# Optimization experiments

Measured on AMD Instinct MI355X. Metric: run time of the kernel, lower is better.

## Reference

```python
import jax, jax.numpy as jnp
import numpy as np

G = 32           # number of graphs
NODES = 256      # nodes per graph (equal-sized graphs)
P = 8            # primary capsules per node
IN_DIM = 128     # primary capsule dim
O = 16           # out_caps
OUT_DIM = 128    # out capsule dim
SDIM = OUT_DIM // 2
V = 16           # vector channels
R = 3            # routing iterations


def squash(t, axis=-1):
    sn = jnp.sum(t * t, axis=axis, keepdims=True)
    scale = sn / (1.0 + sn)
    return scale * t / (jnp.sqrt(sn) + 1e-8)


def setup_inputs() -> dict:
    key = jax.random.key(0)
    ks = jax.random.split(key, 4)
    N = G * NODES
    x = jax.random.normal(ks[0], (N, P, IN_DIM), dtype=jnp.float32)
    x_vectors = jax.random.normal(ks[1], (N, V, 3), dtype=jnp.float32)
    W_scalar = jax.random.normal(ks[2], (O, IN_DIM // 2, SDIM), dtype=jnp.float32)
    W_vector = jax.random.normal(ks[3], (O, IN_DIM // 2, OUT_DIM - SDIM), dtype=jnp.float32)
    bias = jnp.zeros((O, OUT_DIM), dtype=jnp.float32)
    batch = jnp.repeat(jnp.arange(G, dtype=jnp.int64), NODES)  # contiguous equal-size graphs
    return {"x": x, "x_vectors": x_vectors, "W_scalar": W_scalar,
            "W_vector": W_vector, "bias": bias, "batch": batch}


def reference(x, x_vectors, W_scalar, W_vector, bias, batch):
    # Equal-size contiguous graphs -> per-graph masking == reshape to [G, NODES, ...]
    xg = x.reshape(G, NODES, P, IN_DIM)
    xvg = x_vectors.reshape(G, NODES, V, 3)

    def per_graph(xb, xvb):
        scalar_part = xb[..., : IN_DIM // 2]           # [n, P, D/2]
        vector_part = xb[..., IN_DIM // 2:]
        u_s = jnp.einsum('npd,ods->npos', scalar_part, W_scalar)
        u_v = jnp.einsum('npd,odv->npov', vector_part, W_vector)
        u = jnp.concatenate([u_s, u_v], axis=-1).reshape(NODES * P, O, OUT_DIM)

        b = jnp.zeros((NODES * P, O), dtype=xb.dtype)
        c = None
        v = None
        for it in range(R):
            c = jax.nn.softmax(b, axis=1)                     # [M, O]
            s_j = jnp.einsum('mo,mod->od', c, u) + bias       # [O, OUT_DIM]
            v = squash(s_j, axis=1)
            if it < R - 1:
                agreement = jnp.einsum('mos,os->mo', u[..., :SDIM], v[:, :SDIM])
                b = b + agreement

        cr = c.reshape(NODES, P, O)
        routed = jnp.einsum('npo,nvc->ovc', cr, xvb)          # [O, V, 3]
        return v, routed

    caps, vecs = jax.vmap(per_graph)(xg, xvg)
    return caps, vecs
```

## Files before the change

### kernel.cpp

```cpp
#include <hip/hip_runtime.h>

#define G_    32
#define O_    16
#define OUTD  128
#define DS_   64
#define VC    48
#define M_    2048
#define ROWS  128
#define CPG   16
#define XP    136
#define XPD   68
#define WVP   72
#define XNP   72
#define YLP   132

typedef __attribute__((ext_vector_type(8))) short short8;
typedef __attribute__((ext_vector_type(4))) float f32x4;
typedef unsigned long long u64_t;

__device__ __forceinline__ unsigned short f2bf(float f) {
  unsigned u = __float_as_uint(f);
  return (unsigned short)((u + 0x7FFFu + ((u >> 16) & 1u)) >> 16);
}
__device__ __forceinline__ float bf2f(short v) {
  return __uint_as_float(((unsigned)(unsigned short)v) << 16);
}
__device__ __forceinline__ unsigned cvtpk(float lo, float hi) {
  unsigned r;
  asm("v_cvt_pk_bf16_f32 %0, %1, %2" : "=v"(r) : "v"(lo), "v"(hi));
  return r;
}

__device__ __forceinline__ void st8f(float* p, float a, float b) {
  union { float f[2]; u64_t u; } x; x.f[0] = a; x.f[1] = b;
  __hip_atomic_store((u64_t*)p, x.u, __ATOMIC_RELAXED, __HIP_MEMORY_SCOPE_AGENT);
}
__device__ __forceinline__ void ld8f(const float* p, float& a, float& b) {
  union { float f[2]; u64_t u; } x;
  x.u = __hip_atomic_load((const u64_t*)p, __ATOMIC_RELAXED, __HIP_MEMORY_SCOPE_AGENT);
  a = x.f[0]; b = x.f[1];
}

__device__ __forceinline__ void graph_barrier(unsigned* cnt, unsigned target) {
  asm volatile("s_waitcnt vmcnt(0)" ::: "memory");
  __syncthreads();
  if (threadIdx.x == 0) {
    __hip_atomic_fetch_add(cnt, 1u, __ATOMIC_RELAXED, __HIP_MEMORY_SCOPE_AGENT);
    unsigned guard = 0;
    while (__hip_atomic_load(cnt, __ATOMIC_RELAXED, __HIP_MEMORY_SCOPE_AGENT) < target) {
      __builtin_amdgcn_s_sleep(1);
      if (++guard > (1u << 20)) break;
    }
  }
  __syncthreads();
}

__global__ __launch_bounds__(512) void caps_mega7(
    const float* __restrict__ x, const float* __restrict__ xv,
    const float* __restrict__ Ws, const float* __restrict__ Wv,
    const float* __restrict__ bias, short* __restrict__ wvacc_bf,
    float* __restrict__ y_part, float* __restrict__ routed_part,
    float* __restrict__ ysum_part, float* __restrict__ caps,
    float* __restrict__ vecs, unsigned* __restrict__ bar)
{
  const int b = blockIdx.x, g = b >> 4, chunk = b & 15;
  const int t = threadIdx.x;
  const int lane = t & 63, w = t >> 6;

  __shared__ short xT[128 * XP];
  __shared__ short xN[128 * XNP];
  __shared__ short cT[O_ * XP];
  __shared__ short wv_s[O_ * WVP];
  __shared__ float y_lds[16 * YLP];
  __shared__ float cp_s[16][17];
  __shared__ float xv_s[16 * VC];
  __shared__ float yB[128];
  __shared__ float ps[2][128];
  __shared__ float vB[64];
  __shared__ float pn_s[2];
  __shared__ float wv_acc_s[64];

  unsigned* cnt = bar + g * 64;

  {
    const float* xg = x + (size_t)b * (ROWS * OUTD);
    const int rg = lane, c16 = w;
    const float* r0 = xg + (size_t)(2 * rg) * OUTD + c16 * 16;
    const float* r1 = r0 + OUTD;
    const float4* r0q = (const float4*)r0;
    const float4* r1q = (const float4*)r1;
    float4 a0 = r0q[0], a1 = r0q[1], a2 = r0q[2], a3 = r0q[3];
    float4 b0 = r1q[0], b1 = r1q[1], b2 = r1q[2], b3 = r1q[3];
    unsigned pk[16];
    pk[ 0] = cvtpk(a0.x, b0.x); pk[ 1] = cvtpk(a0.y, b0.y);
    pk[ 2] = cvtpk(a0.z, b0.z); pk[ 3] = cvtpk(a0.w, b0.w);
    pk[ 4] = cvtpk(a1.x, b1.x); pk[ 5] = cvtpk(a1.y, b1.y);
    pk[ 6] = cvtpk(a1.z, b1.z); pk[ 7] = cvtpk(a1.w, b1.w);
    pk[ 8] = cvtpk(a2.x, b2.x); pk[ 9] = cvtpk(a2.y, b2.y);
    pk[10] = cvtpk(a2.z, b2.z); pk[11] = cvtpk(a2.w, b2.w);
    pk[12] = cvtpk(a3.x, b3.x); pk[13] = cvtpk(a3.y, b3.y);
    pk[14] = cvtpk(a3.z, b3.z); pk[15] = cvtpk(a3.w, b3.w);
    unsigned* xTd = (unsigned*)xT;
    const int kb = c16 * 16;
#pragma unroll
    for (int i = 0; i < 16; ++i) xTd[(kb + i) * XPD + rg] = pk[i];
    if (c16 < 4) {
      union { unsigned u[4]; short8 s; } pA, pB;
#pragma unroll
      for (int j = 0; j < 4; ++j) {
        pA.u[j] = (pk[2*j] & 0xFFFFu) | (pk[2*j+1] << 16);
        pB.u[j] = (pk[2*j] >> 16) | (pk[2*j+1] & 0xFFFF0000u);
      }
      *(short8*)&xN[(2 * rg) * XNP + kb]     = pA.s;
      *(short8*)&xN[(2 * rg + 1) * XNP + kb] = pB.s;
#pragma unroll
      for (int j = 0; j < 4; ++j) {
        pA.u[j] = (pk[8+2*j] & 0xFFFFu) | (pk[8+2*j+1] << 16);
        pB.u[j] = (pk[8+2*j] >> 16) | (pk[8+2*j+1] & 0xFFFF0000u);
      }
      *(short8*)&xN[(2 * rg) * XNP + kb + 8]     = pA.s;
      *(short8*)&xN[(2 * rg + 1) * XNP + kb + 8] = pB.s;
    }
    float cs[16];
#pragma unroll
    for (int i = 0; i < 16; ++i)
      cs[i] = bf2f((short)(pk[i] & 0xFFFF)) + bf2f((short)(pk[i] >> 16));
#pragma unroll
    for (int i = 0; i < 16; ++i) {
      cs[i] += __shfl_xor(cs[i], 1);
      cs[i] += __shfl_xor(cs[i], 2);
      cs[i] += __shfl_xor(cs[i], 4);
      cs[i] += __shfl_xor(cs[i], 8);
      cs[i] += __shfl_xor(cs[i], 16);
      cs[i] += __shfl_xor(cs[i], 32);
    }
    if (lane == 0) {
#pragma unroll
      for (int i = 0; i < 8; ++i)
        st8f(&ysum_part[(size_t)b * 128 + kb + 2 * i], cs[2*i], cs[2*i+1]);
    }
  }
  {
    const float* xvg = xv + (size_t)(g * 256 + chunk * 16) * VC;
    for (int i = t; i < 16 * VC; i += 512) xv_s[i] = xvg[i];
  }
  graph_barrier(cnt, 16);

#define A_ROLE(LASTF)                                                          \
  {                                                                            \
    if (t < 256) {                                                             \
      u64_t v4 = __hip_atomic_load(                                            \
          (const u64_t*)&wvacc_bf[(size_t)g * 1024 + t * 4],                   \
          __ATOMIC_RELAXED, __HIP_MEMORY_SCOPE_AGENT);                         \
      const int o = t >> 4, k = (t * 4) & 63;                                  \
      wv_s[o * WVP + k + 0] = (short)(v4 & 0xFFFF);                            \
      wv_s[o * WVP + k + 1] = (short)((v4 >> 16) & 0xFFFF);                    \
      wv_s[o * WVP + k + 2] = (short)((v4 >> 32) & 0xFFFF);                    \
      wv_s[o * WVP + k + 3] = (short)((v4 >> 48) & 0xFFFF);                    \
    }                                                                          \
    __syncthreads();                                                           \
          \
    { const int mrow = lane & 15, gq = lane >> 4;                              \
      const int nt = w;                                                        \
      const int mcol = nt * 16 + mrow;                                         \
      f32x4 acc = {0.f, 0.f, 0.f, 0.f};                                        \
      _Pragma("unroll")                                                        \
      for (int ks = 0; ks < 2; ++ks) {                                         \
        short8 af = *(const short8*)&wv_s[mrow * WVP + ks * 32 + gq * 8];      \
        short8 bfr = *(const short8*)&xN[mcol * XNP + ks * 32 + gq * 8];       \
        acc = __builtin_amdgcn_mfma_f32_16x16x32_bf16(af, bfr, acc, 0, 0, 0);  \
      }                                                                        \
      float mx = fmaxf(fmaxf(acc[0], acc[1]), fmaxf(acc[2], acc[3]));          \
      mx = fmaxf(mx, __shfl_xor(mx, 16));                                      \
      mx = fmaxf(mx, __shfl_xor(mx, 32));                                      \
      float e0 = __expf(acc[0] - mx), e1 = __expf(acc[1] - mx);                \
      float e2 = __expf(acc[2] - mx), e3 = __expf(acc[3] - mx);                \
      float sm = e0 + e1 + e2 + e3;                                            \
      sm += __shfl_xor(sm, 16);                                                \
      sm += __shfl_xor(sm, 32);                                                \
      float inv = 1.f / sm;                                                    \
      float c0 = e0 * inv, c1 = e1 * inv, c2 = e2 * inv, c3 = e3 * inv;        \
      cT[(gq * 4 + 0) * XP + mcol] = (short)f2bf(c0);                          \
      cT[(gq * 4 + 1) * XP + mcol] = (short)f2bf(c1);                          \
      cT[(gq * 4 + 2) * XP + mcol] = (short)f2bf(c2);                          \
      cT[(gq * 4 + 3) * XP + mcol] = (short)f2bf(c3);                          \
      if (LASTF) {                                                             \
        float cf[4] = {c0, c1, c2, c3};                                        \
        _Pragma("unroll")                                                      \
        for (int r = 0; r < 4; ++r) {                                          \
          float v = cf[r];                                                     \
          v += __shfl_xor(v, 1); v += __shfl_xor(v, 2); v += __shfl_xor(v, 4); \
          if ((lane & 7) == 0)                                                 \
            cp_s[nt * 2 + ((lane >> 3) & 1)][gq * 4 + r] = v;                  \
        }                                                                      \
      } }                                                                      \
    __syncthreads();                                                           \
                                              \
    { const int oc = lane & 15, gq = lane >> 4;                                \
      f32x4 y0 = {0.f,0.f,0.f,0.f};                                            \
      _Pragma("unroll")                                                        \
      for (int ks = 0; ks < 4; ++ks) {                                         \
        short8 bfv = *(const short8*)&cT[oc * XP + ks * 32 + gq * 8];          \
        short8 av = *(const short8*)&xT[(w * 16 + oc) * XP + ks * 32 + gq * 8];\
        y0 = __builtin_amdgcn_mfma_f32_16x16x32_bf16(av, bfv, y0, 0, 0, 0);    \
      }                                                                        \
      _Pragma("unroll")                                                        \
      for (int r = 0; r < 4; ++r)                                              \
        y_lds[oc * YLP + w * 16 + gq * 4 + r] = y0[r]; }                       \
    __syncthreads();                                                           \
    { float* yp = y_part + (size_t)b * 2048;                                   \
      const int oo = t >> 5, kk = (t * 4) & 127;                               \
      const float* sp = &y_lds[oo * YLP + kk];                                 \
      st8f(&yp[t * 4], sp[0], sp[1]);                                          \
      st8f(&yp[t * 4 + 2], sp[2], sp[3]); }                                    \
    if (LASTF) {                                                               \
      if (t < 384) {                                                           \
        float* rp = routed_part + (size_t)b * 768;                             \
        const int idx0 = 2 * t;                                                \
        const int o = idx0 / VC, j = idx0 - o * VC;                            \
        float a0 = 0.f, a1 = 0.f;                                              \
        _Pragma("unroll")                                                      \
        for (int n = 0; n < 16; ++n) {                                         \
          a0 += cp_s[n][o] * xv_s[n * VC + j];                                 \
          a1 += cp_s[n][o] * xv_s[n * VC + j + 1];                             \
        }                                                                      \
        st8f(&rp[idx0], a0, a1);                                               \
      } }                                                                      \
  }

#define B_ROLE(FIRSTF, LASTF)                                                  \
  {                                                                            \
    const int o = chunk;                                                       \
    if (t < 64) {                                                              \
      float s0 = 0.f, s1 = 0.f;                                                \
      if (FIRSTF) {                                                            \
        _Pragma("unroll")                                                      \
        for (int ch = 0; ch < CPG; ++ch) {                                     \
          float a, bb;                                                         \
          ld8f(&ysum_part[(size_t)(g * CPG + ch) * 128 + 2 * t], a, bb);       \
          s0 += a; s1 += bb;                                                   \
        }                                                                      \
        s0 *= 0.0625f; s1 *= 0.0625f;                                          \
      } else {                                                                 \
        const float* yp = y_part + (size_t)g * CPG * 2048 + o * 128 + 2 * t;   \
        _Pragma("unroll")                                                      \
        for (int ch = 0; ch < CPG; ++ch) {                                     \
          float a, bb; ld8f(&yp[ch * 2048], a, bb);                            \
          s0 += a; s1 += bb;                                                   \
        }                                                                      \
      }                                                                        \
      yB[2*t] = s0; yB[2*t+1] = s1;                                            \
    }                                                                          \
    __syncthreads();                                                           \
    if (t < 256) {          \
      const int kh = t >> 7, d = t & 127;                                      \
      const float* W = (d < 64) ? (Ws + (size_t)o * 4096 + d)                  \
                                : (Wv + (size_t)o * 4096 + (d - 64));          \
      const int ybase = (d < 64) ? 0 : 64;                                     \
      float a0 = 0.f, a1 = 0.f;                                                \
      _Pragma("unroll")                                                        \
      for (int k = 0; k < 32; k += 2) {                                        \
        const int kl = kh * 32 + k;                                            \
        a0 += yB[ybase + kl] * W[(size_t)kl * 64];                             \
        a1 += yB[ybase + kl + 1] * W[(size_t)(kl + 1) * 64];                   \
      }                                                                        \
      ps[kh][d] = a0 + a1;                                                     \
    }                                                                          \
    __syncthreads();                                                           \
    float sv = 0.f;                                                            \
    if (t < 128) {                                                             \
      sv = ps[0][t] + ps[1][t] + bias[o * OUTD + t];                           \
      float pn = sv * sv;                                                      \
      _Pragma("unroll")                                                        \
      for (int m = 1; m < 64; m <<= 1) pn += __shfl_xor(pn, m);                \
      if ((t & 63) == 0) pn_s[t >> 6] = pn;                                    \
    }                                                                          \
    __syncthreads();                                                           \
    if (t < 128) {                                                             \
      float sn = pn_s[0] + pn_s[1];                                            \
      float f = sn / ((1.f + sn) * (sqrtf(sn) + 1e-8f));                       \
      float v = f * sv;                                                        \
      if (t < 64) vB[t] = v;                                                   \
      if (LASTF) caps[((size_t)g * O_ + o) * OUTD + t] = v;                    \
    }                                                                          \
    __syncthreads();                                                           \
    if (!(LASTF)) {                                                            \
      if (t < 128) {              \
        const int k = t >> 1, half = t & 1;                                    \
        const float* Wr = Ws + ((size_t)o * 64 + k) * 64 + half * 32;          \
        float acc = 0.f;                                                       \
        _Pragma("unroll")                                                      \
        for (int ss = 0; ss < 32; ss += 4) {                                   \
          float4 wq = *(const float4*)(Wr + ss);                               \
          float4 vq = *(const float4*)&vB[half * 32 + ss];                     \
          acc += wq.x*vq.x + wq.y*vq.y + wq.z*vq.z + wq.w*vq.w;                \
        }                                                                      \
        acc += __shfl_xor(acc, 1);                                             \
        if (half == 0)                                                         \
          wv_acc_s[k] = ((FIRSTF) ? 0.f : wv_acc_s[k]) + acc;                  \
      }                                                                        \
      __syncthreads();                                                         \
      if (t < 16) {        \
        const int k = t * 4;                                                   \
        u64_t v4 =  (u64_t)(unsigned short)f2bf(wv_acc_s[k + 0])               \
                 | ((u64_t)(unsigned short)f2bf(wv_acc_s[k + 1]) << 16)        \
                 | ((u64_t)(unsigned short)f2bf(wv_acc_s[k + 2]) << 32)        \
                 | ((u64_t)(unsigned short)f2bf(wv_acc_s[k + 3]) << 48);       \
        __hip_atomic_store(                                                    \
            (u64_t*)&wvacc_bf[(size_t)g * 1024 + o * 64 + k],                  \
            v4, __ATOMIC_RELAXED, __HIP_MEMORY_SCOPE_AGENT);                   \
      }                                                                        \
    } else {                                                                   \
      if (t < 24) {                                                            \
        const int idx = o * VC + 2 * t;                                        \
        const float* rp = routed_part + (size_t)g * CPG * 768 + idx;           \
        float s0 = 0.f, s1 = 0.f;                                              \
        _Pragma("unroll")                                                      \
        for (int ch = 0; ch < CPG; ++ch) {                                     \
          float a, bb; ld8f(&rp[ch * 768], a, bb);                             \
          s0 += a; s1 += bb;                                                   \
        }                                                                      \
        vecs[(size_t)g * 768 + idx] = s0;                                      \
        vecs[(size_t)g * 768 + idx + 1] = s1;                                  \
      }                                                                        \
    }                                                                          \
  }

  B_ROLE(1, 0)
  graph_barrier(cnt, 32);
  A_ROLE(0)
  graph_barrier(cnt, 48);
  B_ROLE(0, 0)
  graph_barrier(cnt, 64);
  A_ROLE(1)
  graph_barrier(cnt, 80);
  B_ROLE(0, 1)

#undef A_ROLE
#undef B_ROLE
}

extern "C" void kernel_launch(void* const* d_in, const int* in_sizes, int n_in,
                              void* d_out, int out_size, void* d_ws, size_t ws_size,
                              hipStream_t stream)
{
  const float* x    = (const float*)d_in[0];
  const float* xv   = (const float*)d_in[1];
  const float* Ws   = (const float*)d_in[2];
  const float* Wv   = (const float*)d_in[3];
  const float* bias = (const float*)d_in[4];

  float* out  = (float*)d_out;
  float* caps = out;
  float* vecs = out + (size_t)G_ * O_ * OUTD;

  float* ws          = (float*)d_ws;
  unsigned* bar      = (unsigned*)ws;
  float* ysum_part   = ws + 4096;
  float* y_part      = ysum_part + (size_t)G_ * CPG * 128;
  float* routed_part = y_part + (size_t)G_ * CPG * 2048;
  short* wvacc_bf    = (short*)(routed_part + (size_t)G_ * CPG * 768);

  hipMemsetAsync((void*)bar, 0, (size_t)G_ * 64 * sizeof(unsigned), stream);
  caps_mega7<<<dim3(G_ * CPG), dim3(512), 0, stream>>>(
      x, xv, Ws, Wv, bias, wvacc_bf, y_part, routed_part, ysum_part,
      caps, vecs, bar);
}
```

Before: 40.52 us.

## Split into staging kernel and two-block-per-graph routing kernel

Replaces the single 512-block cooperative kernel, which used five per-graph global barriers across 16 blocks, with two kernels. A staging kernel converts x to bf16 transposed and normal layouts and writes them to global memory along with column sums. A routing kernel then runs 2 blocks of 1024 threads per graph. Each block reloads the staged tiles and keeps the routing state in LDS, and the two blocks exchange partial sums through global memory with a two-party barrier. This cuts barrier participants and drops the cross-block atomic reductions, but it adds a global round-trip of the staged bf16 data, a second launch, and much less parallelism (64 blocks).

```diff
diff --git a/kernel.cpp b/kernel.cpp
--- a/kernel.cpp
+++ b/kernel.cpp
@@ -12,8 +12,6 @@
 #define XPD   68
 #define WVP   72
 #define XNP   72
-#define YLP   132
-
 typedef __attribute__((ext_vector_type(8))) short short8;
 typedef __attribute__((ext_vector_type(4))) float f32x4;
 typedef unsigned long long u64_t;
@@ -30,7 +28,6 @@
   asm("v_cvt_pk_bf16_f32 %0, %1, %2" : "=v"(r) : "v"(lo), "v"(hi));
   return r;
 }
-
 __device__ __forceinline__ void st8f(float* p, float a, float b) {
   union { float f[2]; u64_t u; } x; x.f[0] = a; x.f[1] = b;
   __hip_atomic_store((u64_t*)p, x.u, __ATOMIC_RELAXED, __HIP_MEMORY_SCOPE_AGENT);
@@ -40,7 +37,6 @@
   x.u = __hip_atomic_load((const u64_t*)p, __ATOMIC_RELAXED, __HIP_MEMORY_SCOPE_AGENT);
   a = x.f[0]; b = x.f[1];
 }
-
 __device__ __forceinline__ void graph_barrier(unsigned* cnt, unsigned target) {
   asm volatile("s_waitcnt vmcnt(0)" ::: "memory");
   __syncthreads();
@@ -55,40 +51,20 @@
   __syncthreads();
 }
 
-__global__ __launch_bounds__(512) void caps_mega7(
-    const float* __restrict__ x, const float* __restrict__ xv,
-    const float* __restrict__ Ws, const float* __restrict__ Wv,
-    const float* __restrict__ bias, short* __restrict__ wvacc_bf,
-    float* __restrict__ y_part, float* __restrict__ routed_part,
-    float* __restrict__ ysum_part, float* __restrict__ caps,
-    float* __restrict__ vecs, unsigned* __restrict__ bar)
+__global__ __launch_bounds__(512) void stage_k(
+    const float* __restrict__ x, short* __restrict__ xTg,
+    short* __restrict__ xNg, float* __restrict__ ysum_part)
 {
-  const int b = blockIdx.x, g = b >> 4, chunk = b & 15;
-  const int t = threadIdx.x;
+  const int b = blockIdx.x, t = threadIdx.x;
   const int lane = t & 63, w = t >> 6;
-
   __shared__ short xT[128 * XP];
   __shared__ short xN[128 * XNP];
-  __shared__ short cT[O_ * XP];
-  __shared__ short wv_s[O_ * WVP];
-  __shared__ float y_lds[16 * YLP];
-  __shared__ float cp_s[16][17];
-  __shared__ float xv_s[16 * VC];
-  __shared__ float yB[128];
-  __shared__ float ps[2][128];
-  __shared__ float vB[64];
-  __shared__ float pn_s[2];
-  __shared__ float wv_acc_s[64];
-
-  unsigned* cnt = bar + g * 64;
 
   {
     const float* xg = x + (size_t)b * (ROWS * OUTD);
     const int rg = lane, c16 = w;
-    const float* r0 = xg + (size_t)(2 * rg) * OUTD + c16 * 16;
-    const float* r1 = r0 + OUTD;
-    const float4* r0q = (const float4*)r0;
-    const float4* r1q = (const float4*)r1;
+    const float4* r0q = (const float4*)(xg + (size_t)(2 * rg) * OUTD + c16 * 16);
+    const float4* r1q = (const float4*)(xg + (size_t)(2 * rg + 1) * OUTD + c16 * 16);
     float4 a0 = r0q[0], a1 = r0q[1], a2 = r0q[2], a3 = r0q[3];
     float4 b0 = r1q[0], b1 = r1q[1], b2 = r1q[2], b3 = r1q[3];
     unsigned pk[16];
@@ -127,217 +103,241 @@
       cs[i] = bf2f((short)(pk[i] & 0xFFFF)) + bf2f((short)(pk[i] >> 16));
 #pragma unroll
     for (int i = 0; i < 16; ++i) {
-      cs[i] += __shfl_xor(cs[i], 1);
-      cs[i] += __shfl_xor(cs[i], 2);
-      cs[i] += __shfl_xor(cs[i], 4);
-      cs[i] += __shfl_xor(cs[i], 8);
-      cs[i] += __shfl_xor(cs[i], 16);
-      cs[i] += __shfl_xor(cs[i], 32);
+      cs[i] += __shfl_xor(cs[i], 1);  cs[i] += __shfl_xor(cs[i], 2);
+      cs[i] += __shfl_xor(cs[i], 4);  cs[i] += __shfl_xor(cs[i], 8);
+      cs[i] += __shfl_xor(cs[i], 16); cs[i] += __shfl_xor(cs[i], 32);
     }
     if (lane == 0) {
 #pragma unroll
-      for (int i = 0; i < 8; ++i)
-        st8f(&ysum_part[(size_t)b * 128 + kb + 2 * i], cs[2*i], cs[2*i+1]);
-    }
-  }
+      for (int i = 0; i < 4; ++i) {
+        float4 q = {cs[4*i], cs[4*i+1], cs[4*i+2], cs[4*i+3]};
+        *(float4*)&ysum_part[(size_t)b * 128 + kb + 4 * i] = q;
+      }
+    }
+  }
+  __syncthreads();
   {
-    const float* xvg = xv + (size_t)(g * 256 + chunk * 16) * VC;
-    for (int i = t; i < 16 * VC; i += 512) xv_s[i] = xvg[i];
-  }
-  graph_barrier(cnt, 16);
-
-#define A_ROLE(LASTF)                                                          \
+    short8* dst = (short8*)(xTg + (size_t)b * 16384);
+#pragma unroll
+    for (int i = 0; i < 4; ++i) {
+      int c = i * 512 + t;
+      dst[c] = *(const short8*)&xT[(c >> 4) * XP + (c & 15) * 8];
+    }
+    short8* dn = (short8*)(xNg + (size_t)b * 8192);
+#pragma unroll
+    for (int i = 0; i < 2; ++i) {
+      int c = i * 512 + t;
+      dn[c] = *(const short8*)&xN[(c >> 3) * XNP + (c & 7) * 8];
+    }
+  }
+}
+
+__global__ __launch_bounds__(1024) void route_k(
+    const short* __restrict__ xTg, const short* __restrict__ xNg,
+    const float* __restrict__ xv, const float* __restrict__ Ws,
+    const float* __restrict__ Wv, const float* __restrict__ bias,
+    const float* __restrict__ ysum_part, float* __restrict__ exch,
+    float* __restrict__ caps, float* __restrict__ vecs,
+    unsigned* __restrict__ bar)
+{
+  const int r = blockIdx.x, g = r >> 1, half = r & 1;
+  const int t = threadIdx.x, hw = t >> 9, tl = t & 511;
+  const int lane = t & 63, w8 = tl >> 6;
+
+  __shared__ short xT[2][128 * XP];
+  __shared__ short xN[2][128 * XNP];
+  __shared__ short cT[2][O_ * XP];
+  __shared__ short wv_s[O_ * WVP];
+  __shared__ float yacc[2][16][130];
+  __shared__ float racc[2][768];
+  __shared__ float cp_s[2][16][17];
+  __shared__ float xv_s[2][16 * VC];
+  __shared__ float csum[128];
+  __shared__ float vB[16][64];
+  __shared__ float wvA[16][64];
+
+  unsigned* cnt = bar + g * 16;
+  const size_t exmine = ((size_t)g * 2 + half) * 2816;
+  const size_t exoth  = ((size_t)g * 2 + (1 - half)) * 2816;
+
+  if (t < 128) {
+    float s = 0.f;
+#pragma unroll
+    for (int ch = 0; ch < CPG; ++ch)
+      s += ysum_part[(size_t)(g * CPG + ch) * 128 + t];
+    csum[t] = s * 0.0625f;
+  }
+  __syncthreads();
+
+#define B_COMPUTE(FIRSTF, LASTF)                                               \
   {                                                                            \
-    if (t < 256) {                                                             \
-      u64_t v4 = __hip_atomic_load(                                            \
-          (const u64_t*)&wvacc_bf[(size_t)g * 1024 + t * 4],                   \
-          __ATOMIC_RELAXED, __HIP_MEMORY_SCOPE_AGENT);                         \
-      const int o = t >> 4, k = (t * 4) & 63;                                  \
-      wv_s[o * WVP + k + 0] = (short)(v4 & 0xFFFF);                            \
-      wv_s[o * WVP + k + 1] = (short)((v4 >> 16) & 0xFFFF);                    \
-      wv_s[o * WVP + k + 2] = (short)((v4 >> 32) & 0xFFFF);                    \
-      wv_s[o * WVP + k + 3] = (short)((v4 >> 48) & 0xFFFF);                    \
+    const int o = t >> 6, dd = t & 63;                                         \
+    float s0 = 0.f, s1 = 0.f;                                                  \
+    const float* Wsp = Ws + (size_t)o * 4096 + dd;                             \
+    const float* Wvp = Wv + (size_t)o * 4096 + dd;                             \
+    _Pragma("unroll 8")                                                        \
+    for (int k = 0; k < 64; ++k) {                                             \
+      float y0k = (FIRSTF) ? csum[k]      : yacc[0][o][k];                     \
+      float y1k = (FIRSTF) ? csum[64 + k] : yacc[0][o][64 + k];                \
+      s0 += y0k * Wsp[(size_t)k * 64];                                         \
+      s1 += y1k * Wvp[(size_t)k * 64];                                         \
+    }                                                                          \
+    s0 += bias[o * OUTD + dd];                                                 \
+    s1 += bias[o * OUTD + 64 + dd];                                            \
+    float pn = s0 * s0 + s1 * s1;                                              \
+    _Pragma("unroll")                                                          \
+    for (int m = 1; m < 64; m <<= 1) pn += __shfl_xor(pn, m);                  \
+    float f = pn / ((1.f + pn) * (sqrtf(pn) + 1e-8f));                         \
+    float v0 = f * s0, v1 = f * s1;                                            \
+    vB[o][dd] = v0;                                                            \
+    if ((LASTF) && ((o < 8) == (half == 0))) {                                 \
+      caps[((size_t)g * O_ + o) * OUTD + dd] = v0;                             \
+      caps[((size_t)g * O_ + o) * OUTD + 64 + dd] = v1;                        \
     }                                                                          \
     __syncthreads();                                                           \
-          \
-    { const int mrow = lane & 15, gq = lane >> 4;                              \
-      const int nt = w;                                                        \
-      const int mcol = nt * 16 + mrow;                                         \
-      f32x4 acc = {0.f, 0.f, 0.f, 0.f};                                        \
+    if (!(LASTF)) {                                                            \
+      const float* Wr = Ws + ((size_t)o * 64 + dd) * 64;                       \
+      float acc = 0.f;                                                         \
       _Pragma("unroll")                                                        \
-      for (int ks = 0; ks < 2; ++ks) {                                         \
-        short8 af = *(const short8*)&wv_s[mrow * WVP + ks * 32 + gq * 8];      \
-        short8 bfr = *(const short8*)&xN[mcol * XNP + ks * 32 + gq * 8];       \
-        acc = __builtin_amdgcn_mfma_f32_16x16x32_bf16(af, bfr, acc, 0, 0, 0);  \
+      for (int ss = 0; ss < 64; ss += 4) {                                     \
+        float4 wq = *(const float4*)(Wr + ss);                                 \
+        float4 vq = *(const float4*)&vB[o][ss];                                \
+        acc += wq.x * vq.x + wq.y * vq.y + wq.z * vq.z + wq.w * vq.w;          \
       }                                                                        \
-      float mx = fmaxf(fmaxf(acc[0], acc[1]), fmaxf(acc[2], acc[3]));          \
-      mx = fmaxf(mx, __shfl_xor(mx, 16));                                      \
-      mx = fmaxf(mx, __shfl_xor(mx, 32));                                      \
-      float e0 = __expf(acc[0] - mx), e1 = __expf(acc[1] - mx);                \
-      float e2 = __expf(acc[2] - mx), e3 = __expf(acc[3] - mx);                \
-      float sm = e0 + e1 + e2 + e3;                                            \
-      sm += __shfl_xor(sm, 16);                                                \
-      sm += __shfl_xor(sm, 32);                                                \
-      float inv = 1.f / sm;                                                    \
-      float c0 = e0 * inv, c1 = e1 * inv, c2 = e2 * inv, c3 = e3 * inv;        \
-      cT[(gq * 4 + 0) * XP + mcol] = (short)f2bf(c0);                          \
-      cT[(gq * 4 + 1) * XP + mcol] = (short)f2bf(c1);                          \
-      cT[(gq * 4 + 2) * XP + mcol] = (short)f2bf(c2);                          \
-      cT[(gq * 4 + 3) * XP + mcol] = (short)f2bf(c3);                          \
+      float nw = ((FIRSTF) ? 0.f : wvA[o][dd]) + acc;                          \
+      wvA[o][dd] = nw;                                                         \
+      wv_s[o * WVP + dd] = (short)f2bf(nw);                                    \
+      __syncthreads();                                                         \
+    }                                                                          \
+  }
+
+#define A_ITER(LASTF, TARGET)                                                  \
+  {                                                                            \
+                        \
+    _Pragma("unroll")                                                          \
+    for (int i = 0; i < 2; ++i) {                                              \
+      int e = i * 2048 + t * 2;                                                \
+      yacc[e >> 11][(e >> 7) & 15][e & 127] = 0.f;                             \
+      yacc[e >> 11][(e >> 7) & 15][(e & 127) + 1] = 0.f;                       \
+    }                                                                          \
+    if (LASTF) { if (t < 768) { racc[0][t] = 0.f; racc[1][t] = 0.f; } }        \
+    __syncthreads();                                                           \
+    for (int s = 0; s < 4; ++s) {                                              \
+      const int chunk = half * 8 + s * 2 + hw;                                 \
+      { const short8* srcT = (const short8*)(xTg + (size_t)(g*16+chunk)*16384);\
+        _Pragma("unroll")                                                      \
+        for (int i = 0; i < 4; ++i) {                                          \
+          int c = i * 512 + tl;                                                \
+          *(short8*)&xT[hw][(c >> 4) * XP + (c & 15) * 8] = srcT[c];           \
+        }                                                                      \
+        const short8* srcN = (const short8*)(xNg + (size_t)(g*16+chunk)*8192); \
+        _Pragma("unroll")                                                      \
+        for (int i = 0; i < 2; ++i) {                                          \
+          int c = i * 512 + tl;                                                \
+          *(short8*)&xN[hw][(c >> 3) * XNP + (c & 7) * 8] = srcN[c];           \
+        } }                                                                    \
       if (LASTF) {                                                             \
-        float cf[4] = {c0, c1, c2, c3};                                        \
-        _Pragma("unroll")                                                      \
-        for (int r = 0; r < 4; ++r) {                                          \
-          float v = cf[r];                                                     \
-          v += __shfl_xor(v, 1); v += __shfl_xor(v, 2); v += __shfl_xor(v, 4); \
-          if ((lane & 7) == 0)                                                 \
-            cp_s[nt * 2 + ((lane >> 3) & 1)][gq * 4 + r] = v;                  \
+        const float* xvg = xv + (size_t)(g * 256 + chunk * 16) * VC;           \
+        for (int i = tl; i < 16 * VC; i += 512) xv_s[hw][i] = xvg[i];          \
+      }                                                                        \
+      __syncthreads();                                                         \
+                                          \
+      { const int mrow = lane & 15, gq = lane >> 4;                            \
+        const int mcol = w8 * 16 + mrow;                                       \
+        f32x4 acc = {0.f, 0.f, 0.f, 0.f};                                      \
+        _Pragma("unroll")                                                      \
+        for (int ks = 0; ks < 2; ++ks) {                                       \
+          short8 af = *(const short8*)&wv_s[mrow * WVP + ks * 32 + gq * 8];    \
+          short8 bfr = *(const short8*)&xN[hw][mcol * XNP + ks * 32 + gq * 8]; \
+          acc = __builtin_amdgcn_mfma_f32_16x16x32_bf16(af, bfr, acc, 0,0,0);  \
         }                                                                      \
-      } }                                                                      \
-    __syncthreads();                                                           \
+        float mx = fmaxf(fmaxf(acc[0], acc[1]), fmaxf(acc[2], acc[3]));        \
+        mx = fmaxf(mx, __shfl_xor(mx, 16));                                    \
+        mx = fmaxf(mx, __shfl_xor(mx, 32));                                    \
+        float e0 = __expf(acc[0]-mx), e1 = __expf(acc[1]-mx);                  \
+        float e2 = __expf(acc[2]-mx), e3 = __expf(acc[3]-mx);                  \
+        float sm = e0 + e1 + e2 + e3;                                          \
+        sm += __shfl_xor(sm, 16); sm += __shfl_xor(sm, 32);                    \
+        float inv = 1.f / sm;                                                  \
+        float c0 = e0*inv, c1 = e1*inv, c2 = e2*inv, c3 = e3*inv;              \
+        cT[hw][(gq*4+0)*XP + mcol] = (short)f2bf(c0);                          \
+        cT[hw][(gq*4+1)*XP + mcol] = (short)f2bf(c1);                          \
+        cT[hw][(gq*4+2)*XP + mcol] = (short)f2bf(c2);                          \
+        cT[hw][(gq*4+3)*XP + mcol] = (short)f2bf(c3);                          \
+        if (LASTF) {                                                           \
+          float cf[4] = {c0, c1, c2, c3};                                      \
+          _Pragma("unroll")                                                    \
+          for (int rr = 0; rr < 4; ++rr) {                                     \
+            float v = cf[rr];                                                  \
+            v += __shfl_xor(v, 1); v += __shfl_xor(v, 2); v += __shfl_xor(v,4);\
+            if ((lane & 7) == 0)                                               \
+              cp_s[hw][w8 * 2 + ((lane >> 3) & 1)][gq * 4 + rr] = v;           \
+          }                                                                    \
+        } }                                                                    \
+      __syncthreads();                                                         \
+                                           \
+      { const int oc = lane & 15, gq = lane >> 4;                              \
+        f32x4 y0 = {0.f, 0.f, 0.f, 0.f};                                       \
+        _Pragma("unroll")                                                      \
+        for (int ks = 0; ks < 4; ++ks) {                                       \
+          short8 bfv = *(const short8*)&cT[hw][oc * XP + ks * 32 + gq * 8];    \
+          short8 av = *(const short8*)&xT[hw][(w8*16+oc)*XP + ks*32 + gq*8];   \
+          y0 = __builtin_amdgcn_mfma_f32_16x16x32_bf16(av, bfv, y0, 0, 0, 0);  \
+        }                                                                      \
+        _Pragma("unroll")                                                      \
+        for (int rr = 0; rr < 4; ++rr)                                         \
+          yacc[hw][oc][w8 * 16 + gq * 4 + rr] += y0[rr]; }                     \
+      if (LASTF) {                                                             \
+        if (tl < 384) {                                                        \
+          const int idx0 = 2 * tl;                                             \
+          const int o = idx0 / VC, j = idx0 - o * VC;                          \
+          float a0 = 0.f, a1 = 0.f;                                            \
+          _Pragma("unroll")                                                    \
+          for (int n = 0; n < 16; ++n) {                                       \
+            a0 += cp_s[hw][n][o] * xv_s[hw][n * VC + j];                       \
+            a1 += cp_s[hw][n][o] * xv_s[hw][n * VC + j + 1];                   \
+          }                                                                    \
+          racc[hw][idx0] += a0; racc[hw][idx0 + 1] += a1;                      \
+        } }                                                                    \
+      __syncthreads();                                                         \
+    }                                                                          \
                                               \
-    { const int oc = lane & 15, gq = lane >> 4;                                \
-      f32x4 y0 = {0.f,0.f,0.f,0.f};                                            \
-      _Pragma("unroll")                                                        \
-      for (int ks = 0; ks < 4; ++ks) {                                         \
-        short8 bfv = *(const short8*)&cT[oc * XP + ks * 32 + gq * 8];          \
-        short8 av = *(const short8*)&xT[(w * 16 + oc) * XP + ks * 32 + gq * 8];\
-        y0 = __builtin_amdgcn_mfma_f32_16x16x32_bf16(av, bfv, y0, 0, 0, 0);    \
-      }                                                                        \
-      _Pragma("unroll")                                                        \
-      for (int r = 0; r < 4; ++r)                                              \
-        y_lds[oc * YLP + w * 16 + gq * 4 + r] = y0[r]; }                       \
-    __syncthreads();                                                           \
-    { float* yp = y_part + (size_t)b * 2048;                                   \
-      const int oo = t >> 5, kk = (t * 4) & 127;                               \
-      const float* sp = &y_lds[oo * YLP + kk];                                 \
-      st8f(&yp[t * 4], sp[0], sp[1]);                                          \
-      st8f(&yp[t * 4 + 2], sp[2], sp[3]); }                                    \
+    { const int e2 = t * 2, o = e2 >> 7, k = e2 & 127;                         \
+      float m0 = yacc[0][o][k] + yacc[1][o][k];                                \
+      float m1 = yacc[0][o][k + 1] + yacc[1][o][k + 1];                        \
+      yacc[0][o][k] = m0; yacc[0][o][k + 1] = m1;                              \
+      st8f(&exch[exmine + e2], m0, m1); }                                      \
     if (LASTF) {                                                               \
       if (t < 384) {                                                           \
-        float* rp = routed_part + (size_t)b * 768;                             \
         const int idx0 = 2 * t;                                                \
-        const int o = idx0 / VC, j = idx0 - o * VC;                            \
-        float a0 = 0.f, a1 = 0.f;                                              \
-        _Pragma("unroll")                                                      \
-        for (int n = 0; n < 16; ++n) {                                         \
-          a0 += cp_s[n][o] * xv_s[n * VC + j];                                 \
-          a1 += cp_s[n][o] * xv_s[n * VC + j + 1];                             \
-        }                                                                      \
-        st8f(&rp[idx0], a0, a1);                                               \
+        float r0 = racc[0][idx0] + racc[1][idx0];                              \
+        float r1 = racc[0][idx0 + 1] + racc[1][idx0 + 1];                      \
+        racc[0][idx0] = r0; racc[0][idx0 + 1] = r1;                            \
+        st8f(&exch[exmine + 2048 + idx0], r0, r1);                             \
       } }                                                                      \
-  }
-
-#define B_ROLE(FIRSTF, LASTF)                                                  \
-  {                                                                            \
-    const int o = chunk;                                                       \
-    if (t < 64) {                                                              \
-      float s0 = 0.f, s1 = 0.f;                                                \
-      if (FIRSTF) {                                                            \
-        _Pragma("unroll")                                                      \
-        for (int ch = 0; ch < CPG; ++ch) {                                     \
-          float a, bb;                                                         \
-          ld8f(&ysum_part[(size_t)(g * CPG + ch) * 128 + 2 * t], a, bb);       \
-          s0 += a; s1 += bb;                                                   \
-        }                                                                      \
-        s0 *= 0.0625f; s1 *= 0.0625f;                                          \
-      } else {                                                                 \
-        const float* yp = y_part + (size_t)g * CPG * 2048 + o * 128 + 2 * t;   \
-        _Pragma("unroll")                                                      \
-        for (int ch = 0; ch < CPG; ++ch) {                                     \
-          float a, bb; ld8f(&yp[ch * 2048], a, bb);                            \
-          s0 += a; s1 += bb;                                                   \
-        }                                                                      \
-      }                                                                        \
-      yB[2*t] = s0; yB[2*t+1] = s1;                                            \
-    }                                                                          \
+    graph_barrier(cnt, TARGET);                                                \
+    { const int e2 = t * 2, o = e2 >> 7, k = e2 & 127;                         \
+      float a, b2; ld8f(&exch[exoth + e2], a, b2);                             \
+      yacc[0][o][k] += a; yacc[0][o][k + 1] += b2; }                           \
     __syncthreads();                                                           \
-    if (t < 256) {          \
-      const int kh = t >> 7, d = t & 127;                                      \
-      const float* W = (d < 64) ? (Ws + (size_t)o * 4096 + d)                  \
-                                : (Wv + (size_t)o * 4096 + (d - 64));          \
-      const int ybase = (d < 64) ? 0 : 64;                                     \
-      float a0 = 0.f, a1 = 0.f;                                                \
-      _Pragma("unroll")                                                        \
-      for (int k = 0; k < 32; k += 2) {                                        \
-        const int kl = kh * 32 + k;                                            \
-        a0 += yB[ybase + kl] * W[(size_t)kl * 64];                             \
-        a1 += yB[ybase + kl + 1] * W[(size_t)(kl + 1) * 64];                   \
-      }                                                                        \
-      ps[kh][d] = a0 + a1;                                                     \
-    }                                                                          \
-    __syncthreads();                                                           \
-    float sv = 0.f;                                                            \
-    if (t < 128) {                                                             \
-      sv = ps[0][t] + ps[1][t] + bias[o * OUTD + t];                           \
-      float pn = sv * sv;                                                      \
-      _Pragma("unroll")                                                        \
-      for (int m = 1; m < 64; m <<= 1) pn += __shfl_xor(pn, m);                \
-      if ((t & 63) == 0) pn_s[t >> 6] = pn;                                    \
-    }                                                                          \
-    __syncthreads();                                                           \
-    if (t < 128) {                                                             \
-      float sn = pn_s[0] + pn_s[1];                                            \
-      float f = sn / ((1.f + sn) * (sqrtf(sn) + 1e-8f));                       \
-      float v = f * sv;                                                        \
-      if (t < 64) vB[t] = v;                                                   \
-      if (LASTF) caps[((size_t)g * O_ + o) * OUTD + t] = v;                    \
-    }                                                                          \
-    __syncthreads();                                                           \
-    if (!(LASTF)) {                                                            \
-      if (t < 128) {              \
-        const int k = t >> 1, half = t & 1;                                    \
-        const float* Wr = Ws + ((size_t)o * 64 + k) * 64 + half * 32;          \
-        float acc = 0.f;                                                       \
-        _Pragma("unroll")                                                      \
-        for (int ss = 0; ss < 32; ss += 4) {                                   \
-          float4 wq = *(const float4*)(Wr + ss);                               \
-          float4 vq = *(const float4*)&vB[half * 32 + ss];                     \
-          acc += wq.x*vq.x + wq.y*vq.y + wq.z*vq.z + wq.w*vq.w;                \
-        }                                                                      \
-        acc += __shfl_xor(acc, 1);                                             \
-        if (half == 0)                                                         \
-          wv_acc_s[k] = ((FIRSTF) ? 0.f : wv_acc_s[k]) + acc;                  \
-      }                                                                        \
-      __syncthreads();                                                         \
-      if (t < 16) {        \
-        const int k = t * 4;                                                   \
-        u64_t v4 =  (u64_t)(unsigned short)f2bf(wv_acc_s[k + 0])               \
-                 | ((u64_t)(unsigned short)f2bf(wv_acc_s[k + 1]) << 16)        \
-                 | ((u64_t)(unsigned short)f2bf(wv_acc_s[k + 2]) << 32)        \
-                 | ((u64_t)(unsigned short)f2bf(wv_acc_s[k + 3]) << 48);       \
-        __hip_atomic_store(                                                    \
-            (u64_t*)&wvacc_bf[(size_t)g * 1024 + o * 64 + k],                  \
-            v4, __ATOMIC_RELAXED, __HIP_MEMORY_SCOPE_AGENT);                   \
-      }                                                                        \
-    } else {                                                                   \
-      if (t < 24) {                                                            \
-        const int idx = o * VC + 2 * t;                                        \
-        const float* rp = routed_part + (size_t)g * CPG * 768 + idx;           \
-        float s0 = 0.f, s1 = 0.f;                                              \
-        _Pragma("unroll")                                                      \
-        for (int ch = 0; ch < CPG; ++ch) {                                     \
-          float a, bb; ld8f(&rp[ch * 768], a, bb);                             \
-          s0 += a; s1 += bb;                                                   \
-        }                                                                      \
-        vecs[(size_t)g * 768 + idx] = s0;                                      \
-        vecs[(size_t)g * 768 + idx + 1] = s1;                                  \
-      }                                                                        \
-    }                                                                          \
-  }
-
-  B_ROLE(1, 0)
-  graph_barrier(cnt, 32);
-  A_ROLE(0)
-  graph_barrier(cnt, 48);
-  B_ROLE(0, 0)
-  graph_barrier(cnt, 64);
-  A_ROLE(1)
-  graph_barrier(cnt, 80);
-  B_ROLE(0, 1)
-
-#undef A_ROLE
-#undef B_ROLE
+  }
+
+  B_COMPUTE(1, 0)
+  A_ITER(0, 2)
+  B_COMPUTE(0, 0)
+  A_ITER(1, 4)
+  B_COMPUTE(0, 1)
+  if (t < 384) {
+    const int idx0 = 2 * t;
+    float a, b2; ld8f(&exch[exoth + 2048 + idx0], a, b2);
+    float v0 = racc[0][idx0] + a, v1 = racc[0][idx0 + 1] + b2;
+    if ((idx0 < 384) == (half == 0)) {
+      vecs[(size_t)g * 768 + idx0] = v0;
+      vecs[(size_t)g * 768 + idx0 + 1] = v1;
+    }
+  }
+#undef A_ITER
+#undef B_COMPUTE
 }
 
 extern "C" void kernel_launch(void* const* d_in, const int* in_sizes, int n_in,
@@ -354,15 +354,15 @@
   float* caps = out;
   float* vecs = out + (size_t)G_ * O_ * OUTD;
 
-  float* ws          = (float*)d_ws;
-  unsigned* bar      = (unsigned*)ws;
-  float* ysum_part   = ws + 4096;
-  float* y_part      = ysum_part + (size_t)G_ * CPG * 128;
-  float* routed_part = y_part + (size_t)G_ * CPG * 2048;
-  short* wvacc_bf    = (short*)(routed_part + (size_t)G_ * CPG * 768);
-
-  hipMemsetAsync((void*)bar, 0, (size_t)G_ * 64 * sizeof(unsigned), stream);
-  caps_mega7<<<dim3(G_ * CPG), dim3(512), 0, stream>>>(
-      x, xv, Ws, Wv, bias, wvacc_bf, y_part, routed_part, ysum_part,
-      caps, vecs, bar);
-}
+  float* ws        = (float*)d_ws;
+  unsigned* bar    = (unsigned*)ws;
+  float* ysum_part = ws + 2048;
+  float* exch      = ysum_part + 65536;
+  short* xTg       = (short*)(exch + 180224);
+  short* xNg       = xTg + (size_t)8388608;
+
+  hipMemsetAsync((void*)bar, 0, 8192, stream);
+  stage_k<<<dim3(G_ * CPG), dim3(512), 0, stream>>>(x, xTg, xNg, ysum_part);
+  route_k<<<dim3(G_ * 2), dim3(1024), 0, stream>>>(
+      xTg, xNg, xv, Ws, Wv, bias, ysum_part, exch, caps, vecs, bar);
+}
```

Result: slower. 84.39 us (+108.3%).
